# Optimization experiments

Hardware: AMD Instinct MI355X
Metric: run time of the kernel (lower is better)

## Reference

```python
import jax, jax.numpy as jnp
import numpy as np

B, S, FEAT, HID, H = 8, 1024, 1024, 1024, 8
DH = HID // H  # head dim = 128
MASK_VAL = -128.0  # mask_val = -2**7 (soft additive mask, per original code)


def setup_inputs() -> dict:
    key = jax.random.key(0)
    ks = jax.random.split(key, 4)
    scale = 0.02
    return {
        "queries": jax.random.normal(ks[0], (B, S, FEAT), dtype=jnp.float32),
        "Wq": jax.random.normal(ks[1], (FEAT, HID), dtype=jnp.float32) * scale,
        "bq": jnp.zeros((HID,), dtype=jnp.float32),
        "Wk": jax.random.normal(ks[2], (FEAT, HID), dtype=jnp.float32) * scale,
        "bk": jnp.zeros((HID,), dtype=jnp.float32),
        "Wv": jax.random.normal(ks[3], (FEAT, HID), dtype=jnp.float32) * scale,
        "bv": jnp.zeros((HID,), dtype=jnp.float32),
    }


def reference(queries, Wq, bq, Wk, bk, Wv, bv):
    # Self-attention: keys = values = queries (torch forward defaults)
    q = queries @ Wq + bq  # [B,S,HID]
    k = queries @ Wk + bk
    v = queries @ Wv + bv
    # split heads: chunk along last dim == reshape (B,S,H,DH)
    qh = q.reshape(B, S, H, DH)
    kh = k.reshape(B, S, H, DH)
    vh = v.reshape(B, S, H, DH)
    # exp-scaled-dot score (non-standard: exp BEFORE mask/softmax)
    logits = jnp.einsum("bqhd,bkhd->bhqk", qh, kh) / np.float32(np.sqrt(DH))
    score = jnp.exp(logits)
    # soft additive causal mask: upper triangle (diag=1) gets -128
    mask = jnp.triu(jnp.full((S, S), MASK_VAL, dtype=score.dtype), k=1)
    att = jax.nn.softmax(score + mask, axis=-1)  # [B,H,S,S]
    ctx = jnp.einsum("bhqk,bkhd->bqhd", att, vh)  # [B,S,H,DH]
    # reverse heads: concat along last dim
    return ctx.reshape(B, S, HID)
```

## Files before the change

### kernel.cpp

```cpp
#include <hip/hip_runtime.h>


typedef __bf16 bf16x8 __attribute__((ext_vector_type(8)));
typedef float floatx4 __attribute__((ext_vector_type(4)));
typedef unsigned short u16;
typedef unsigned int u32;

#define RSCALE 0.08838834764831845f

__device__ __forceinline__ u16 f2b(float f) {
  union { float f; unsigned u; } v; v.f = f;
  return (u16)((v.u + 0x7FFFu + ((v.u >> 16) & 1u)) >> 16);
}

__device__ __forceinline__ void gld_lds16(const void* g, void* l) {
  __builtin_amdgcn_global_load_lds(
      (const __attribute__((address_space(1))) unsigned*)g,
      (__attribute__((address_space(3))) unsigned*)l, 16, 0, 0);
}

#define MFMA16(a, b, c) __builtin_amdgcn_mfma_f32_16x16x32_bf16(a, b, c, 0, 0, 0)

__global__ __launch_bounds__(256) void prep_kernel(
    const float4* __restrict__ X, u16* __restrict__ Xb,
    const float* __restrict__ Wq, const float* __restrict__ Wk,
    const float* __restrict__ Wv, u16* __restrict__ Wtb) {
  if (blockIdx.x < 8192) {
    unsigned i = blockIdx.x * 256u + threadIdx.x;
    float4 v = X[i];
    ushort4 o;
    o.x = f2b(v.x); o.y = f2b(v.y); o.z = f2b(v.z); o.w = f2b(v.w);
    *reinterpret_cast<ushort4*>(Xb + 4u * i) = o;
  } else {
    const int bid = blockIdx.x - 8192;
    const int mat = bid >> 10;
    const int bx = bid & 31, by = (bid >> 5) & 31;
    const float* W = (mat == 0) ? Wq : (mat == 1) ? Wk : Wv;
    u16* Wt = Wtb + (size_t)mat * (1024u * 1024u);
    __shared__ u16 tile[32][33];
    const int x = threadIdx.x & 31, y = threadIdx.x >> 5;
    const int kt = bx * 32, nt = by * 32;
#pragma unroll
    for (int i = 0; i < 4; ++i)
      tile[y + 8 * i][x] = f2b(W[(size_t)(kt + y + 8 * i) * 1024 + nt + x]);
    __syncthreads();
#pragma unroll
    for (int i = 0; i < 4; ++i)
      Wt[(size_t)(nt + y + 8 * i) * 1024 + kt + x] = tile[x][y + 8 * i];
  }
}

__global__ __launch_bounds__(256, 2) void gemm_qkv_kernel(
    const u16* __restrict__ Xb, const u16* __restrict__ Wtb,
    const float* __restrict__ bq, const float* __restrict__ bk,
    const float* __restrict__ bv, u16* __restrict__ Qh, u16* __restrict__ Kh,
    u16* __restrict__ Vt) {
  const int mat = blockIdx.z;
  const u16* __restrict__ Wt = Wtb + (size_t)mat * (1024u * 1024u);
  const float* __restrict__ bias = (mat == 0) ? bq : (mat == 1) ? bk : bv;

  const int m0 = blockIdx.x * 128;
  const int n0 = blockIdx.y * 128;

  __shared__ u16 As[2][128 * 64];
  __shared__ u16 Bs[2][128 * 64];

  const int tid = threadIdx.x;
  const int wid = tid >> 6;
  const int lane = tid & 63;
  const int quad = lane >> 4;
  const int l16 = lane & 15;
  const int wm = (wid & 1) * 64;
  const int wn = (wid >> 1) * 64;

  const floatx4 z4 = {0.f, 0.f, 0.f, 0.f};
  floatx4 acc[4][4];
#pragma unroll
  for (int i = 0; i < 4; ++i)
#pragma unroll
    for (int j = 0; j < 4; ++j) acc[i][j] = z4;

  const int srow = wid * 32;
  const int lrow = lane >> 3;
  const int gblk = (lane & 7) ^ lrow;

  auto stage = [&](int b, int k0) {
#pragma unroll
    for (int c = 0; c < 4; ++c) {
      const int row = srow + c * 8 + lrow;
      gld_lds16(Xb + (size_t)(m0 + row) * 1024 + k0 + gblk * 8,
                As[b] + (srow + c * 8) * 64);
      gld_lds16(Wt + (size_t)(n0 + row) * 1024 + k0 + gblk * 8,
                Bs[b] + (srow + c * 8) * 64);
    }
  };

  stage(0, 0);

  for (int i = 0; i < 16; ++i) {
    __syncthreads();
    if (i < 15) stage((i + 1) & 1, (i + 1) * 64);

    const u16* __restrict__ Ab = As[i & 1];
    const u16* __restrict__ Bb = Bs[i & 1];
#pragma unroll
    for (int c = 0; c < 2; ++c) {
      const int phys = ((c * 4 + quad) ^ (l16 & 7)) * 8;
      bf16x8 af[4], bfr[4];
#pragma unroll
      for (int ii = 0; ii < 4; ++ii)
        af[ii] = *(const bf16x8*)(Ab + (wm + ii * 16 + l16) * 64 + phys);
#pragma unroll
      for (int j = 0; j < 4; ++j)
        bfr[j] = *(const bf16x8*)(Bb + (wn + j * 16 + l16) * 64 + phys);
#pragma unroll
      for (int ii = 0; ii < 4; ++ii)
#pragma unroll
        for (int j = 0; j < 4; ++j)
          acc[ii][j] = MFMA16(af[ii], bfr[j], acc[ii][j]);
    }
  }

  const int b = m0 >> 10;
  const int h = n0 >> 7;
  const int sbase = (m0 & 1023) + wm;
  float bv4[4];
#pragma unroll
  for (int j = 0; j < 4; ++j) bv4[j] = bias[n0 + wn + j * 16 + l16];

  if (mat < 2) {
    u16* outp = (mat == 0 ? Qh : Kh) + (size_t)(b * 8 + h) * 1024 * 128;
#pragma unroll
    for (int i = 0; i < 4; ++i)
#pragma unroll
      for (int j = 0; j < 4; ++j) {
        const int d = wn + j * 16 + l16;
#pragma unroll
        for (int r = 0; r < 4; ++r) {
          const int s = sbase + i * 16 + quad * 4 + r;
          outp[(size_t)s * 128 + d] = f2b(acc[i][j][r] + bv4[j]);
        }
      }
  } else {
    u16* outp = Vt + (size_t)(b * 8 + h) * 128 * 1024;
#pragma unroll
    for (int i = 0; i < 4; ++i)
#pragma unroll
      for (int j = 0; j < 4; ++j) {
        const int d = wn + j * 16 + l16;
        const int s = sbase + i * 16 + quad * 4;
        ushort4 pk;
        pk.x = f2b(acc[i][j][0] + bv4[j]);
        pk.y = f2b(acc[i][j][1] + bv4[j]);
        pk.z = f2b(acc[i][j][2] + bv4[j]);
        pk.w = f2b(acc[i][j][3] + bv4[j]);
        *(ushort4*)(outp + (size_t)d * 1024 + s) = pk;
      }
  }
}

__global__ __launch_bounds__(256, 2) void attn_kernel(const u16* __restrict__ Qh,
                                                      const u16* __restrict__ Kh,
                                                      const u16* __restrict__ Vt,
                                                      float* __restrict__ out) {
  const int id = blockIdx.x;
  const int x = id & 7;
  const int j = id >> 3;
  const int bh = x * 8 + (j & 7);
  const int QTMAP[8] = {7, 5, 6, 4, 0, 2, 1, 3};
  const int qt = QTMAP[j >> 3];
  const int q0 = qt * 128;

  const int tid = threadIdx.x;
  const int wid = tid >> 6;
  const int lane = tid & 63;
  const int quad = lane >> 4;
  const int l16 = lane & 15;

  __shared__ u16 Ks[2][64 * 128];
  __shared__ u16 Vs[2][128 * 64];
  __shared__ u16 Ps[4][32 * 32];

  const u16* __restrict__ Qbase = Qh + (size_t)bh * 1024 * 128;
  const u16* __restrict__ Kbase = Kh + (size_t)bh * 1024 * 128;
  const u16* __restrict__ Vbase = Vt + (size_t)bh * 128 * 1024;

  const int qw = q0 + wid * 32;

  bf16x8 qf[2][4];
#pragma unroll
  for (int nt = 0; nt < 2; ++nt)
#pragma unroll
    for (int c = 0; c < 4; ++c)
      qf[nt][c] = *(const bf16x8*)(Qbase + (size_t)(qw + nt * 16 + l16) * 128 +
                                   c * 32 + quad * 8);

  const floatx4 z4 = {0.f, 0.f, 0.f, 0.f};
  floatx4 o[2][8];
#pragma unroll
  for (int nt = 0; nt < 2; ++nt)
#pragma unroll
    for (int dt = 0; dt < 8; ++dt) o[nt][dt] = z4;
  float lacc[2] = {0.f, 0.f};

  auto stage = [&](int b, int k0) {
#pragma unroll
    for (int c = 0; c < 4; ++c) {
      const int r0 = wid * 16 + c * 4;
      const int row = r0 + quad;
      gld_lds16(Kbase + (size_t)(k0 + row) * 128 + ((l16 ^ (c * 4 + quad)) * 8),
                Ks[b] + r0 * 128);
    }
#pragma unroll
    for (int c = 0; c < 4; ++c) {
      const int r0 = wid * 32 + c * 8;
      const int row = r0 + (lane >> 3);
      gld_lds16(Vbase + (size_t)row * 1024 + k0 +
                    (((lane & 7) ^ ((lane >> 3) & 7)) * 8),
                Vs[b] + r0 * 64);
    }
  };

  const int n = (q0 + 128) >> 6;
  stage(0, 0);

  for (int i = 0; i < n; ++i) {
    const int k0 = i << 6;
    __syncthreads();
    if (i + 1 < n) stage((i + 1) & 1, k0 + 64);

    const u16* __restrict__ Kb = Ks[i & 1];
    const u16* __restrict__ Vb = Vs[i & 1];

#pragma unroll
    for (int half = 0; half < 2; ++half) {
      if (k0 + half * 32 > qw + 31) break;

#pragma unroll
      for (int f2 = 0; f2 < 2; ++f2) {
        const int f = half * 2 + f2;
        bf16x8 kf[4];
#pragma unroll
        for (int c = 0; c < 4; ++c)
          kf[c] = *(const bf16x8*)(Kb + (f * 16 + l16) * 128 +
                                   (((c * 4 + quad) ^ l16) * 8));
        floatx4 st[2];
#pragma unroll
        for (int nt = 0; nt < 2; ++nt) {
          st[nt] = z4;
#pragma unroll
          for (int c = 0; c < 4; ++c) st[nt] = MFMA16(kf[c], qf[nt][c], st[nt]);
        }
        const int kb = k0 + f * 16 + quad * 4;
#pragma unroll
        for (int nt = 0; nt < 2; ++nt) {
          const int qrow = qw + nt * 16 + l16;
          float p[4];
#pragma unroll
          for (int r = 0; r < 4; ++r) {
            const float e = fminf(__expf(st[nt][r] * RSCALE), 85.f);
            p[r] = (kb + r > qrow) ? 0.f : __expf(e);
          }
          lacc[nt] += (p[0] + p[1]) + (p[2] + p[3]);
          uint2 pk;
          pk.x = (u32)f2b(p[0]) | ((u32)f2b(p[1]) << 16);
          pk.y = (u32)f2b(p[2]) | ((u32)f2b(p[3]) << 16);
          *(uint2*)((char*)Ps[wid] + (nt * 16 + l16) * 64 +
                    (((f2 * 2 + (quad >> 1)) ^ (l16 & 3)) * 16) +
                    (quad & 1) * 8) = pk;
        }
      }
      asm volatile("s_waitcnt lgkmcnt(0)" ::: "memory");

      bf16x8 pa[2];
#pragma unroll
      for (int nt = 0; nt < 2; ++nt)
        pa[nt] = *(const bf16x8*)((char*)Ps[wid] + (nt * 16 + l16) * 64 +
                                  ((quad ^ (l16 & 3)) * 16));
#pragma unroll
      for (int dt = 0; dt < 8; ++dt) {
        const bf16x8 vf = *(const bf16x8*)(
            Vb + (dt * 16 + l16) * 64 +
            (((half * 4 + quad) ^ (l16 & 7)) * 8));
        o[0][dt] = MFMA16(vf, pa[0], o[0][dt]);
        o[1][dt] = MFMA16(vf, pa[1], o[1][dt]);
      }
    }
  }

  float linv[2];
#pragma unroll
  for (int nt = 0; nt < 2; ++nt) {
    float s = lacc[nt];
    s += __shfl_xor(s, 16);
    s += __shfl_xor(s, 32);
    linv[nt] = 1.0f / s;
  }

  float* outp = out + (size_t)(bh >> 3) * 1024 * 1024 + (bh & 7) * 128;
#pragma unroll
  for (int nt = 0; nt < 2; ++nt) {
    const int qrow = qw + nt * 16 + l16;
#pragma unroll
    for (int dt = 0; dt < 8; ++dt) {
      float4 v;
      v.x = o[nt][dt][0] * linv[nt];
      v.y = o[nt][dt][1] * linv[nt];
      v.z = o[nt][dt][2] * linv[nt];
      v.w = o[nt][dt][3] * linv[nt];
      *(float4*)(outp + (size_t)qrow * 1024 + dt * 16 + quad * 4) = v;
    }
  }
}

extern "C" void kernel_launch(void* const* d_in, const int* in_sizes, int n_in,
                              void* d_out, int out_size, void* d_ws,
                              size_t ws_size, hipStream_t stream) {
  const float* X = (const float*)d_in[0];
  const float* Wq = (const float*)d_in[1];
  const float* bq = (const float*)d_in[2];
  const float* Wk = (const float*)d_in[3];
  const float* bk = (const float*)d_in[4];
  const float* Wv = (const float*)d_in[5];
  const float* bv = (const float*)d_in[6];
  float* out = (float*)d_out;

  char* ws = (char*)d_ws;
  u16* Xb  = (u16*)(ws);
  u16* Wtb = (u16*)(ws + (16u << 20));
  u16* Qh  = (u16*)(ws + (22u << 20));
  u16* Kh  = (u16*)(ws + (38u << 20));
  u16* Vt  = (u16*)(ws + (54u << 20));

  prep_kernel<<<8192 + 3072, 256, 0, stream>>>((const float4*)X, Xb, Wq, Wk,
                                               Wv, Wtb);
  dim3 gg(64, 8, 3);
  gemm_qkv_kernel<<<gg, 256, 0, stream>>>(Xb, Wtb, bq, bk, bv, Qh, Kh, Vt);
  attn_kernel<<<512, 256, 0, stream>>>(Qh, Kh, Vt, out);
}
```

Before: 198.1 us.

## Rewrite QKV GEMM as 256x256 tiles with 8 waves and interleaved prefetch pipeline

The QKV projection GEMM now uses 512-thread blocks computing 256x256 output tiles over the fused N=3072 weight dimension, launched as a 1D grid with an XCD-aware swizzle. The main loop splits each K-step into four MFMA quarter-phases, with the next tile's A and B halves staged into LDS between them. It uses explicit barriers, vmcnt/lgkmcnt waits and s_setprio so loads overlap the MFMA work. This targets better operand reuse and less exposed memory latency. In exchange it uses more registers and LDS (128KB), which may limit occupancy, and the hand-placed waitcnt counts must be exactly right.

```diff
diff --git a/kernel.cpp b/kernel.cpp
--- a/kernel.cpp
+++ b/kernel.cpp
@@ -20,6 +20,15 @@
 }
 
 #define MFMA16(a, b, c) __builtin_amdgcn_mfma_f32_16x16x32_bf16(a, b, c, 0, 0, 0)
+
+__device__ __forceinline__ void barrier_mem() {
+  asm volatile("" ::: "memory");
+  __builtin_amdgcn_s_barrier();
+  asm volatile("" ::: "memory");
+}
+#define WAIT_LGKM0() asm volatile("s_waitcnt lgkmcnt(0)" ::: "memory")
+#define WAIT_VM4()   asm volatile("s_waitcnt vmcnt(4)" ::: "memory")
+#define WAIT_VM0()   asm volatile("s_waitcnt vmcnt(0)" ::: "memory")
 
 __global__ __launch_bounds__(256) void prep_kernel(
     const float4* __restrict__ X, u16* __restrict__ Xb,
@@ -50,111 +59,190 @@
   }
 }
 
-__global__ __launch_bounds__(256, 2) void gemm_qkv_kernel(
+__global__ __launch_bounds__(512, 2) void gemm_qkv_kernel(
     const u16* __restrict__ Xb, const u16* __restrict__ Wtb,
     const float* __restrict__ bq, const float* __restrict__ bk,
     const float* __restrict__ bv, u16* __restrict__ Qh, u16* __restrict__ Kh,
     u16* __restrict__ Vt) {
-  const int mat = blockIdx.z;
-  const u16* __restrict__ Wt = Wtb + (size_t)mat * (1024u * 1024u);
-  const float* __restrict__ bias = (mat == 0) ? bq : (mat == 1) ? bk : bv;
-
-  const int m0 = blockIdx.x * 128;
-  const int n0 = blockIdx.y * 128;
-
-  __shared__ u16 As[2][128 * 64];
-  __shared__ u16 Bs[2][128 * 64];
+  const int id = blockIdx.x;
+  const int swz = (id & 7) * 48 + (id >> 3);
+  const int m0 = (swz / 12) * 256;
+  const int n0g = (swz % 12) * 256;
+
+  __shared__ u16 As[2][256 * 64];
+  __shared__ u16 Bs[2][256 * 64];
 
   const int tid = threadIdx.x;
   const int wid = tid >> 6;
   const int lane = tid & 63;
   const int quad = lane >> 4;
   const int l16 = lane & 15;
-  const int wm = (wid & 1) * 64;
-  const int wn = (wid >> 1) * 64;
+  const int swzr = l16 & 7;
+  const int wrm = (wid >> 2) * 128;
+  const int wcn = (wid & 3) * 64;
+
+  const int srow = tid >> 3;
+  const int sunit = (tid & 7) ^ (srow & 7);
+
+  auto stageA = [&](int buf, int h, int kk) {
+#pragma unroll
+    for (int c = 0; c < 2; ++c)
+      gld_lds16(
+          Xb + (size_t)(m0 + h * 128 + c * 64 + srow) * 1024 + kk + sunit * 8,
+          &As[buf][(h * 128 + c * 64 + wid * 8) * 64]);
+  };
+  auto stageB = [&](int buf, int h, int kk) {
+#pragma unroll
+    for (int c = 0; c < 2; ++c)
+      gld_lds16(
+          Wtb + (size_t)(n0g + h * 128 + c * 64 + srow) * 1024 + kk + sunit * 8,
+          &Bs[buf][(h * 128 + c * 64 + wid * 8) * 64]);
+  };
 
   const floatx4 z4 = {0.f, 0.f, 0.f, 0.f};
-  floatx4 acc[4][4];
-#pragma unroll
-  for (int i = 0; i < 4; ++i)
+  floatx4 acc[8][4];
+#pragma unroll
+  for (int i = 0; i < 8; ++i)
 #pragma unroll
     for (int j = 0; j < 4; ++j) acc[i][j] = z4;
 
-  const int srow = wid * 32;
-  const int lrow = lane >> 3;
-  const int gblk = (lane & 7) ^ lrow;
-
-  auto stage = [&](int b, int k0) {
-#pragma unroll
-    for (int c = 0; c < 4; ++c) {
-      const int row = srow + c * 8 + lrow;
-      gld_lds16(Xb + (size_t)(m0 + row) * 1024 + k0 + gblk * 8,
-                As[b] + (srow + c * 8) * 64);
-      gld_lds16(Wt + (size_t)(n0 + row) * 1024 + k0 + gblk * 8,
-                Bs[b] + (srow + c * 8) * 64);
-    }
-  };
-
-  stage(0, 0);
-
-  for (int i = 0; i < 16; ++i) {
-    __syncthreads();
-    if (i < 15) stage((i + 1) & 1, (i + 1) * 64);
-
-    const u16* __restrict__ Ab = As[i & 1];
-    const u16* __restrict__ Bb = Bs[i & 1];
-#pragma unroll
-    for (int c = 0; c < 2; ++c) {
-      const int phys = ((c * 4 + quad) ^ (l16 & 7)) * 8;
-      bf16x8 af[4], bfr[4];
-#pragma unroll
-      for (int ii = 0; ii < 4; ++ii)
-        af[ii] = *(const bf16x8*)(Ab + (wm + ii * 16 + l16) * 64 + phys);
-#pragma unroll
-      for (int j = 0; j < 4; ++j)
-        bfr[j] = *(const bf16x8*)(Bb + (wn + j * 16 + l16) * 64 + phys);
-#pragma unroll
-      for (int ii = 0; ii < 4; ++ii)
-#pragma unroll
-        for (int j = 0; j < 4; ++j)
-          acc[ii][j] = MFMA16(af[ii], bfr[j], acc[ii][j]);
-    }
-  }
-
+  bf16x8 aR[4][2];
+  bf16x8 bA[2][2];
+  bf16x8 bB[2][2];
+
+  stageA(0, 0, 0); stageA(0, 1, 0);
+  stageB(0, 0, 0); stageB(0, 1, 0);
+  stageB(1, 0, 64); stageB(1, 1, 64);
+  WAIT_VM4();
+  barrier_mem();
+
+#pragma unroll 1
+  for (int t = 0; t < 16; ++t) {
+    const u16* __restrict__ Ab = As[t & 1];
+    const u16* __restrict__ Bb = Bs[t & 1];
+    const int nb = (t + 1) & 1;
+
+#pragma unroll
+    for (int i = 0; i < 4; ++i)
+#pragma unroll
+      for (int c = 0; c < 2; ++c)
+        aR[i][c] = *(const bf16x8*)(Ab + (wrm + i * 16 + l16) * 64 +
+                                    (((c * 4 + quad) ^ swzr) * 8));
+#pragma unroll
+    for (int j = 0; j < 2; ++j)
+#pragma unroll
+      for (int c = 0; c < 2; ++c)
+        bA[j][c] = *(const bf16x8*)(Bb + (wcn + j * 16 + l16) * 64 +
+                                    (((c * 4 + quad) ^ swzr) * 8));
+    if (t < 15) stageA(nb, 0, (t + 1) * 64);
+    barrier_mem();
+    WAIT_LGKM0();
+    __builtin_amdgcn_s_setprio(1);
+#pragma unroll
+    for (int c = 0; c < 2; ++c)
+#pragma unroll
+      for (int i = 0; i < 4; ++i)
+#pragma unroll
+        for (int j = 0; j < 2; ++j)
+          acc[i][j] = MFMA16(aR[i][c], bA[j][c], acc[i][j]);
+    __builtin_amdgcn_s_setprio(0);
+    barrier_mem();
+
+#pragma unroll
+    for (int j = 0; j < 2; ++j)
+#pragma unroll
+      for (int c = 0; c < 2; ++c)
+        bB[j][c] = *(const bf16x8*)(Bb + (wcn + 32 + j * 16 + l16) * 64 +
+                                    (((c * 4 + quad) ^ swzr) * 8));
+    if (t < 15) stageA(nb, 1, (t + 1) * 64);
+    barrier_mem();
+    WAIT_LGKM0();
+    __builtin_amdgcn_s_setprio(1);
+#pragma unroll
+    for (int c = 0; c < 2; ++c)
+#pragma unroll
+      for (int i = 0; i < 4; ++i)
+#pragma unroll
+        for (int j = 0; j < 2; ++j)
+          acc[i][2 + j] = MFMA16(aR[i][c], bB[j][c], acc[i][2 + j]);
+    __builtin_amdgcn_s_setprio(0);
+    barrier_mem();
+
+#pragma unroll
+    for (int i = 0; i < 4; ++i)
+#pragma unroll
+      for (int c = 0; c < 2; ++c)
+        aR[i][c] = *(const bf16x8*)(Ab + (wrm + 64 + i * 16 + l16) * 64 +
+                                    (((c * 4 + quad) ^ swzr) * 8));
+    if (t < 14) stageB(t & 1, 0, (t + 2) * 64);
+    barrier_mem();
+    WAIT_LGKM0();
+    __builtin_amdgcn_s_setprio(1);
+#pragma unroll
+    for (int c = 0; c < 2; ++c)
+#pragma unroll
+      for (int i = 0; i < 4; ++i)
+#pragma unroll
+        for (int j = 0; j < 2; ++j)
+          acc[4 + i][2 + j] = MFMA16(aR[i][c], bB[j][c], acc[4 + i][2 + j]);
+    __builtin_amdgcn_s_setprio(0);
+    barrier_mem();
+
+    if (t < 14) stageB(t & 1, 1, (t + 2) * 64);
+    barrier_mem();
+    WAIT_LGKM0();
+    __builtin_amdgcn_s_setprio(1);
+#pragma unroll
+    for (int c = 0; c < 2; ++c)
+#pragma unroll
+      for (int i = 0; i < 4; ++i)
+#pragma unroll
+        for (int j = 0; j < 2; ++j)
+          acc[4 + i][j] = MFMA16(aR[i][c], bA[j][c], acc[4 + i][j]);
+    __builtin_amdgcn_s_setprio(0);
+    if (t < 14) { WAIT_VM4(); }
+    else if (t == 14) { WAIT_VM0(); }
+    barrier_mem();
+  }
+
+  const int mat = n0g >> 10;
+  const int nn = n0g & 1023;
+  const float* __restrict__ bias = (mat == 0) ? bq : (mat == 1) ? bk : bv;
   const int b = m0 >> 10;
-  const int h = n0 >> 7;
-  const int sbase = (m0 & 1023) + wm;
-  float bv4[4];
-#pragma unroll
-  for (int j = 0; j < 4; ++j) bv4[j] = bias[n0 + wn + j * 16 + l16];
+  const int sbase = (m0 & 1023) + wrm;
+  float bias4[4];
+#pragma unroll
+  for (int j = 0; j < 4; ++j) bias4[j] = bias[nn + wcn + j * 16 + l16];
 
   if (mat < 2) {
-    u16* outp = (mat == 0 ? Qh : Kh) + (size_t)(b * 8 + h) * 1024 * 128;
-#pragma unroll
-    for (int i = 0; i < 4; ++i)
+    u16* outp = (mat == 0 ? Qh : Kh) + (size_t)b * 8 * 1024 * 128;
+#pragma unroll
+    for (int fi = 0; fi < 8; ++fi)
 #pragma unroll
       for (int j = 0; j < 4; ++j) {
-        const int d = wn + j * 16 + l16;
-#pragma unroll
-        for (int r = 0; r < 4; ++r) {
-          const int s = sbase + i * 16 + quad * 4 + r;
-          outp[(size_t)s * 128 + d] = f2b(acc[i][j][r] + bv4[j]);
-        }
+        const int dg = nn + wcn + j * 16 + l16;
+        const int h = dg >> 7, d = dg & 127;
+        const int s = sbase + fi * 16 + quad * 4;
+        u16* p = outp + (size_t)h * 1024 * 128 + (size_t)s * 128 + d;
+#pragma unroll
+        for (int r = 0; r < 4; ++r)
+          p[(size_t)r * 128] = f2b(acc[fi][j][r] + bias4[j]);
       }
   } else {
-    u16* outp = Vt + (size_t)(b * 8 + h) * 128 * 1024;
-#pragma unroll
-    for (int i = 0; i < 4; ++i)
+    u16* outp = Vt + (size_t)b * 8 * 128 * 1024;
+#pragma unroll
+    for (int fi = 0; fi < 8; ++fi)
 #pragma unroll
       for (int j = 0; j < 4; ++j) {
-        const int d = wn + j * 16 + l16;
-        const int s = sbase + i * 16 + quad * 4;
+        const int dg = nn + wcn + j * 16 + l16;
+        const int h = dg >> 7, d = dg & 127;
+        const int s = sbase + fi * 16 + quad * 4;
         ushort4 pk;
-        pk.x = f2b(acc[i][j][0] + bv4[j]);
-        pk.y = f2b(acc[i][j][1] + bv4[j]);
-        pk.z = f2b(acc[i][j][2] + bv4[j]);
-        pk.w = f2b(acc[i][j][3] + bv4[j]);
-        *(ushort4*)(outp + (size_t)d * 1024 + s) = pk;
+        pk.x = f2b(acc[fi][j][0] + bias4[j]);
+        pk.y = f2b(acc[fi][j][1] + bias4[j]);
+        pk.z = f2b(acc[fi][j][2] + bias4[j]);
+        pk.w = f2b(acc[fi][j][3] + bias4[j]);
+        *(ushort4*)(outp + (size_t)h * 128 * 1024 + (size_t)d * 1024 + s) = pk;
       }
   }
 }
@@ -334,7 +422,6 @@
 
   prep_kernel<<<8192 + 3072, 256, 0, stream>>>((const float4*)X, Xb, Wq, Wk,
                                                Wv, Wtb);
-  dim3 gg(64, 8, 3);
-  gemm_qkv_kernel<<<gg, 256, 0, stream>>>(Xb, Wtb, bq, bk, bv, Qh, Kh, Vt);
+  gemm_qkv_kernel<<<384, 512, 0, stream>>>(Xb, Wtb, bq, bk, bv, Qh, Kh, Vt);
   attn_kernel<<<512, 256, 0, stream>>>(Qh, Kh, Vt, out);
 }
```

New measurement: 206.9 us. 1.04x slower.

## Load K/V fragments directly from global memory instead of LDS double buffering

Applied to the files above, without the earlier changes.

Removes the shared-memory K and V staging buffers, their async global-to-LDS copies and the per-iteration block barrier, so each wave reads its K and V MFMA fragments straight from global memory (relying on L2/L1 reuse). It also raises wave priority around the MFMA sequences with s_setprio. The intent is to cut LDS traffic and synchronisation and to free LDS for occupancy. The cost is redundant global loads across the four waves, which share K/V tiles, and exposed load latency with no prefetch.

```diff
diff --git a/kernel.cpp b/kernel.cpp
--- a/kernel.cpp
+++ b/kernel.cpp
@@ -177,8 +177,6 @@
   const int quad = lane >> 4;
   const int l16 = lane & 15;
 
-  __shared__ u16 Ks[2][64 * 128];
-  __shared__ u16 Vs[2][128 * 64];
   __shared__ u16 Ps[4][32 * 32];
 
   const u16* __restrict__ Qbase = Qh + (size_t)bh * 1024 * 128;
@@ -203,34 +201,11 @@
     for (int dt = 0; dt < 8; ++dt) o[nt][dt] = z4;
   float lacc[2] = {0.f, 0.f};
 
-  auto stage = [&](int b, int k0) {
-#pragma unroll
-    for (int c = 0; c < 4; ++c) {
-      const int r0 = wid * 16 + c * 4;
-      const int row = r0 + quad;
-      gld_lds16(Kbase + (size_t)(k0 + row) * 128 + ((l16 ^ (c * 4 + quad)) * 8),
-                Ks[b] + r0 * 128);
-    }
-#pragma unroll
-    for (int c = 0; c < 4; ++c) {
-      const int r0 = wid * 32 + c * 8;
-      const int row = r0 + (lane >> 3);
-      gld_lds16(Vbase + (size_t)row * 1024 + k0 +
-                    (((lane & 7) ^ ((lane >> 3) & 7)) * 8),
-                Vs[b] + r0 * 64);
-    }
-  };
-
   const int n = (q0 + 128) >> 6;
-  stage(0, 0);
-
+
+#pragma unroll 1
   for (int i = 0; i < n; ++i) {
     const int k0 = i << 6;
-    __syncthreads();
-    if (i + 1 < n) stage((i + 1) & 1, k0 + 64);
-
-    const u16* __restrict__ Kb = Ks[i & 1];
-    const u16* __restrict__ Vb = Vs[i & 1];
 
 #pragma unroll
     for (int half = 0; half < 2; ++half) {
@@ -242,15 +217,17 @@
         bf16x8 kf[4];
 #pragma unroll
         for (int c = 0; c < 4; ++c)
-          kf[c] = *(const bf16x8*)(Kb + (f * 16 + l16) * 128 +
-                                   (((c * 4 + quad) ^ l16) * 8));
+          kf[c] = *(const bf16x8*)(Kbase + (size_t)(k0 + f * 16 + l16) * 128 +
+                                   c * 32 + quad * 8);
         floatx4 st[2];
+        __builtin_amdgcn_s_setprio(1);
 #pragma unroll
         for (int nt = 0; nt < 2; ++nt) {
           st[nt] = z4;
 #pragma unroll
           for (int c = 0; c < 4; ++c) st[nt] = MFMA16(kf[c], qf[nt][c], st[nt]);
         }
+        __builtin_amdgcn_s_setprio(0);
         const int kb = k0 + f * 16 + quad * 4;
 #pragma unroll
         for (int nt = 0; nt < 2; ++nt) {
@@ -277,14 +254,15 @@
       for (int nt = 0; nt < 2; ++nt)
         pa[nt] = *(const bf16x8*)((char*)Ps[wid] + (nt * 16 + l16) * 64 +
                                   ((quad ^ (l16 & 3)) * 16));
+      __builtin_amdgcn_s_setprio(1);
 #pragma unroll
       for (int dt = 0; dt < 8; ++dt) {
         const bf16x8 vf = *(const bf16x8*)(
-            Vb + (dt * 16 + l16) * 64 +
-            (((half * 4 + quad) ^ (l16 & 7)) * 8));
+            Vbase + (size_t)(dt * 16 + l16) * 1024 + k0 + half * 32 + quad * 8);
         o[0][dt] = MFMA16(vf, pa[0], o[0][dt]);
         o[1][dt] = MFMA16(vf, pa[1], o[1][dt]);
       }
+      __builtin_amdgcn_s_setprio(0);
     }
   }
 
```

Result: slower. 234.1 us (+18.2%).

## Pair low and high query tiles per block to balance causal attention work

Applied to the files above, without the earlier changes.

Each attention block now handles two 64-row query tiles, p and 15-p, instead of one 128-row tile picked through a fixed order map. Every block therefore does roughly the same number of causal key iterations, which is meant to remove the load imbalance and tail effect across the grid. Per-wave predicates skip the MFMA and exp work for whichever tile is already past its diagonal. The cost is extra branching inside the inner loop. The low tile also still takes part in staging and barriers while it is idle, though it only runs out for the tiles nearest the diagonal.

```diff
diff --git a/kernel.cpp b/kernel.cpp
--- a/kernel.cpp
+++ b/kernel.cpp
@@ -167,9 +167,9 @@
   const int x = id & 7;
   const int j = id >> 3;
   const int bh = x * 8 + (j & 7);
-  const int QTMAP[8] = {7, 5, 6, 4, 0, 2, 1, 3};
-  const int qt = QTMAP[j >> 3];
-  const int q0 = qt * 128;
+  const int p = j >> 3;
+  const int q0L = p * 64;
+  const int q0H = (15 - p) * 64;
 
   const int tid = threadIdx.x;
   const int wid = tid >> 6;
@@ -185,15 +185,18 @@
   const u16* __restrict__ Kbase = Kh + (size_t)bh * 1024 * 128;
   const u16* __restrict__ Vbase = Vt + (size_t)bh * 128 * 1024;
 
-  const int qw = q0 + wid * 32;
+  const int qL = q0L + wid * 16;
+  const int qH = q0H + wid * 16;
 
   bf16x8 qf[2][4];
 #pragma unroll
-  for (int nt = 0; nt < 2; ++nt)
+  for (int nt = 0; nt < 2; ++nt) {
+    const int qb = nt ? qH : qL;
 #pragma unroll
     for (int c = 0; c < 4; ++c)
-      qf[nt][c] = *(const bf16x8*)(Qbase + (size_t)(qw + nt * 16 + l16) * 128 +
+      qf[nt][c] = *(const bf16x8*)(Qbase + (size_t)(qb + l16) * 128 +
                                    c * 32 + quad * 8);
+  }
 
   const floatx4 z4 = {0.f, 0.f, 0.f, 0.f};
   floatx4 o[2][8];
@@ -221,7 +224,7 @@
     }
   };
 
-  const int n = (q0 + 128) >> 6;
+  const int n = 16 - p;
   stage(0, 0);
 
   for (int i = 0; i < n; ++i) {
@@ -234,56 +237,68 @@
 
 #pragma unroll
     for (int half = 0; half < 2; ++half) {
-      if (k0 + half * 32 > qw + 31) break;
-
-#pragma unroll
-      for (int f2 = 0; f2 < 2; ++f2) {
-        const int f = half * 2 + f2;
-        bf16x8 kf[4];
-#pragma unroll
-        for (int c = 0; c < 4; ++c)
-          kf[c] = *(const bf16x8*)(Kb + (f * 16 + l16) * 128 +
-                                   (((c * 4 + quad) ^ l16) * 8));
-        floatx4 st[2];
-#pragma unroll
-        for (int nt = 0; nt < 2; ++nt) {
-          st[nt] = z4;
-#pragma unroll
-          for (int c = 0; c < 4; ++c) st[nt] = MFMA16(kf[c], qf[nt][c], st[nt]);
+      const int kh = k0 + half * 32;
+      const bool aL = (kh <= qL + 15);
+      const bool aH = (kh <= qH + 15);
+      if (aL | aH) {
+#pragma unroll
+        for (int f2 = 0; f2 < 2; ++f2) {
+          const int f = half * 2 + f2;
+          bf16x8 kf[4];
+#pragma unroll
+          for (int c = 0; c < 4; ++c)
+            kf[c] = *(const bf16x8*)(Kb + (f * 16 + l16) * 128 +
+                                     (((c * 4 + quad) ^ l16) * 8));
+          floatx4 st[2];
+          if (aL) {
+            st[0] = z4;
+#pragma unroll
+            for (int c = 0; c < 4; ++c) st[0] = MFMA16(kf[c], qf[0][c], st[0]);
+          }
+          if (aH) {
+            st[1] = z4;
+#pragma unroll
+            for (int c = 0; c < 4; ++c) st[1] = MFMA16(kf[c], qf[1][c], st[1]);
+          }
+          const int kb = k0 + f * 16 + quad * 4;
+#pragma unroll
+          for (int nt = 0; nt < 2; ++nt) {
+            const bool act = nt ? aH : aL;
+            if (act) {
+              const int qrow = (nt ? qH : qL) + l16;
+              float pv[4];
+#pragma unroll
+              for (int r = 0; r < 4; ++r) {
+                const float e = fminf(__expf(st[nt][r] * RSCALE), 85.f);
+                pv[r] = (kb + r > qrow) ? 0.f : __expf(e);
+              }
+              lacc[nt] += (pv[0] + pv[1]) + (pv[2] + pv[3]);
+              uint2 pk;
+              pk.x = (u32)f2b(pv[0]) | ((u32)f2b(pv[1]) << 16);
+              pk.y = (u32)f2b(pv[2]) | ((u32)f2b(pv[3]) << 16);
+              *(uint2*)((char*)Ps[wid] + (nt * 16 + l16) * 64 +
+                        (((f2 * 2 + (quad >> 1)) ^ (l16 & 3)) * 16) +
+                        (quad & 1) * 8) = pk;
+            }
+          }
         }
-        const int kb = k0 + f * 16 + quad * 4;
-#pragma unroll
-        for (int nt = 0; nt < 2; ++nt) {
-          const int qrow = qw + nt * 16 + l16;
-          float p[4];
-#pragma unroll
-          for (int r = 0; r < 4; ++r) {
-            const float e = fminf(__expf(st[nt][r] * RSCALE), 85.f);
-            p[r] = (kb + r > qrow) ? 0.f : __expf(e);
-          }
-          lacc[nt] += (p[0] + p[1]) + (p[2] + p[3]);
-          uint2 pk;
-          pk.x = (u32)f2b(p[0]) | ((u32)f2b(p[1]) << 16);
-          pk.y = (u32)f2b(p[2]) | ((u32)f2b(p[3]) << 16);
-          *(uint2*)((char*)Ps[wid] + (nt * 16 + l16) * 64 +
-                    (((f2 * 2 + (quad >> 1)) ^ (l16 & 3)) * 16) +
-                    (quad & 1) * 8) = pk;
+        asm volatile("s_waitcnt lgkmcnt(0)" ::: "memory");
+
+        bf16x8 pa[2];
+        if (aL)
+          pa[0] = *(const bf16x8*)((char*)Ps[wid] + l16 * 64 +
+                                   ((quad ^ (l16 & 3)) * 16));
+        if (aH)
+          pa[1] = *(const bf16x8*)((char*)Ps[wid] + (16 + l16) * 64 +
+                                   ((quad ^ (l16 & 3)) * 16));
+#pragma unroll
+        for (int dt = 0; dt < 8; ++dt) {
+          const bf16x8 vf = *(const bf16x8*)(
+              Vb + (dt * 16 + l16) * 64 +
+              (((half * 4 + quad) ^ (l16 & 7)) * 8));
+          if (aL) o[0][dt] = MFMA16(vf, pa[0], o[0][dt]);
+          if (aH) o[1][dt] = MFMA16(vf, pa[1], o[1][dt]);
         }
-      }
-      asm volatile("s_waitcnt lgkmcnt(0)" ::: "memory");
-
-      bf16x8 pa[2];
-#pragma unroll
-      for (int nt = 0; nt < 2; ++nt)
-        pa[nt] = *(const bf16x8*)((char*)Ps[wid] + (nt * 16 + l16) * 64 +
-                                  ((quad ^ (l16 & 3)) * 16));
-#pragma unroll
-      for (int dt = 0; dt < 8; ++dt) {
-        const bf16x8 vf = *(const bf16x8*)(
-            Vb + (dt * 16 + l16) * 64 +
-            (((half * 4 + quad) ^ (l16 & 7)) * 8));
-        o[0][dt] = MFMA16(vf, pa[0], o[0][dt]);
-        o[1][dt] = MFMA16(vf, pa[1], o[1][dt]);
       }
     }
   }
@@ -300,7 +315,7 @@
   float* outp = out + (size_t)(bh >> 3) * 1024 * 1024 + (bh & 7) * 128;
 #pragma unroll
   for (int nt = 0; nt < 2; ++nt) {
-    const int qrow = qw + nt * 16 + l16;
+    const int qrow = (nt ? qH : qL) + l16;
 #pragma unroll
     for (int dt = 0; dt < 8; ++dt) {
       float4 v;
```

Result: slower. 202.2 us (+2.0%).
